# Kernel tuning notes

Measured on AMD Instinct MI355X. Metric: run time of the kernel, lower is better.

## Reference

```python
import jax, jax.numpy as jnp
import numpy as np

B, S, D = 2, 2048, 2048
H, KVH = 16, 4
HD = D // H  # 128
ROPE_BASE = 10000.0
EPS = 1e-6
QK_GAIN_INIT = 1.5


def _rms_norm(x):
    var = jnp.mean(jnp.square(x), axis=-1, keepdims=True)
    return x * jax.lax.rsqrt(var + EPS)


def _rope_tables(seqlen, head_dim, dtype):
    half = head_dim // 2
    inv_freq = 1.0 / (ROPE_BASE ** (jnp.arange(0, head_dim, 2, dtype=jnp.float32) / head_dim))
    freqs = jnp.outer(jnp.arange(seqlen, dtype=jnp.float32), inv_freq)  # [S, half]
    return jnp.cos(freqs).astype(dtype)[None, None], jnp.sin(freqs).astype(dtype)[None, None]


def _apply_rotary(x, cos, sin):
    half = x.shape[-1] // 2
    x1, x2 = x[..., :half], x[..., half:]
    return jnp.concatenate((x1 * cos + x2 * sin, -x1 * sin + x2 * cos), axis=-1)


def setup_inputs() -> dict:
    key = jax.random.key(0)
    ks = jax.random.split(key, 5)
    scale = 0.02
    return {
        "x": jax.random.normal(ks[0], (B, S, D), dtype=jnp.float32),
        "Wq": jax.random.normal(ks[1], (D, D), dtype=jnp.float32) * scale,
        "Wk": jax.random.normal(ks[2], (KVH * HD, D), dtype=jnp.float32) * scale,
        "Wv": jax.random.normal(ks[3], (KVH * HD, D), dtype=jnp.float32) * scale,
        "Wproj": jax.random.normal(ks[4], (D, D), dtype=jnp.float32) * scale,
        "q_gain": jnp.full((H,), QK_GAIN_INIT, dtype=jnp.float32),
    }


def reference(x, Wq, Wk, Wv, Wproj, q_gain):
    bsz, seqlen, dim = x.shape
    # QKV projections (torch Linear: y = x @ W.T)
    q = (x @ Wq.T).reshape(bsz, seqlen, H, HD).transpose(0, 2, 1, 3)      # [B,H,S,HD]
    k = (x @ Wk.T).reshape(bsz, seqlen, KVH, HD).transpose(0, 2, 1, 3)    # [B,KVH,S,HD]
    v = (x @ Wv.T).reshape(bsz, seqlen, KVH, HD).transpose(0, 2, 1, 3)
    # QK RMSNorm
    q = _rms_norm(q)
    k = _rms_norm(k)
    # RoPE
    cos, sin = _rope_tables(seqlen, HD, q.dtype)
    q = _apply_rotary(q, cos, sin)
    k = _apply_rotary(k, cos, sin)
    # per-head gain on q
    q = q * q_gain[None, :, None, None]
    # GQA: repeat k/v heads
    n_rep = H // KVH
    k = jnp.repeat(k, n_rep, axis=1)  # [B,H,S,HD]
    v = jnp.repeat(v, n_rep, axis=1)
    # causal SDPA, scale = 1/sqrt(head_dim)
    scores = jnp.einsum("bhqd,bhkd->bhqk", q, k) / jnp.sqrt(jnp.float32(HD))
    causal = jnp.tril(jnp.ones((seqlen, seqlen), dtype=bool))
    scores = jnp.where(causal[None, None], scores, jnp.finfo(scores.dtype).min)
    attn = jax.nn.softmax(scores, axis=-1)
    y = jnp.einsum("bhqk,bhkd->bhqd", attn, v)  # [B,H,S,HD]
    y = y.transpose(0, 2, 1, 3).reshape(bsz, seqlen, dim)
    return y @ Wproj.T
```

## Files before the change

### kernel.cpp

```cpp
#include <hip/hip_runtime.h>
#include <hip/hip_bf16.h>

typedef __attribute__((ext_vector_type(8))) short bf16x8;
typedef __attribute__((ext_vector_type(4))) short bf16x4;
typedef __attribute__((ext_vector_type(4))) float f32x4;
typedef unsigned short u16;

#define B_ 2
#define S_ 2048
#define H_ 16
#define KVH_ 4
#define HD_ 128

__device__ __forceinline__ float bf2f(u16 u) { return __uint_as_float(((unsigned)u) << 16); }
__device__ __forceinline__ u16 f2bf(float f) {
  __hip_bfloat16 h = __float2bfloat16(f);
  return *reinterpret_cast<u16*>(&h);
}
__device__ __forceinline__ void gld16(const void* g, void* l) {
  __builtin_amdgcn_global_load_lds((const __attribute__((address_space(1))) void*)g,
                                   (__attribute__((address_space(3))) void*)l, 16, 0, 0);
}

#define WAITV(n)                                                    \
  do {                                                              \
    asm volatile("s_waitcnt vmcnt(" #n ")" ::: "memory");           \
    __builtin_amdgcn_sched_barrier(0);                              \
  } while (0)

__global__ void detect_kernel(const u16* __restrict__ x, int* __restrict__ flag) {
  __shared__ int tot;
  if (threadIdx.x == 0) tot = 0;
  __syncthreads();
  int cnt = 0;
  for (int i = threadIdx.x; i < 16384; i += 256) {
    unsigned e = (x[i] >> 7) & 0xFF;
    if (e >= 160) cnt++;
  }
  atomicAdd(&tot, cnt);
  __syncthreads();
  if (threadIdx.x == 0) *flag = (tot >= 8) ? 1 : 0;
}

__global__ __launch_bounds__(256) void convert_all_kernel(
    const void* __restrict__ s0, const void* __restrict__ s1, const void* __restrict__ s2,
    const void* __restrict__ s3, const void* __restrict__ s4,
    u16* __restrict__ d0, u16* __restrict__ d1, u16* __restrict__ d2,
    u16* __restrict__ d3, u16* __restrict__ d4, const int* __restrict__ flag) {
  int bb = blockIdx.x;
  const void* src; u16* dst; int base;
  if (bb < 4096)      { src = s0; dst = d0; base = bb; }
  else if (bb < 6144) { src = s1; dst = d1; base = bb - 4096; }
  else if (bb < 6656) { src = s2; dst = d2; base = bb - 6144; }
  else if (bb < 7168) { src = s3; dst = d3; base = bb - 6656; }
  else                { src = s4; dst = d4; base = bb - 7168; }
  int i = (base * 256 + (int)threadIdx.x) * 8;
  if (*flag) {
    const float* s = (const float*)src;
    float4 a = *(const float4*)(s + i);
    float4 b = *(const float4*)(s + i + 4);
    ushort4 o0, o1;
    o0.x = f2bf(a.x); o0.y = f2bf(a.y); o0.z = f2bf(a.z); o0.w = f2bf(a.w);
    o1.x = f2bf(b.x); o1.y = f2bf(b.y); o1.z = f2bf(b.z); o1.w = f2bf(b.w);
    *(ushort4*)(dst + i) = o0;
    *(ushort4*)(dst + i + 4) = o1;
  } else {
    *(uint4*)(dst + i) = *(const uint4*)((const u16*)src + i);
  }
}

__device__ __forceinline__ void stage16(const u16* __restrict__ src, int row0, int K,
                                        int k0, u16* dst, int tid, int wave) {
#pragma unroll
  for (int s = 0; s < 2; ++s) {
    int f = s * 256 + tid, r = f >> 2, kk = (f & 3) << 3;
    gld16(&src[(size_t)(row0 + r) * K + k0 + kk], &dst[(size_t)(s * 256 + wave * 64) * 8]);
  }
}

__device__ __forceinline__ void mfma_tile(const u16* As, const u16* Bs, f32x4 acc[4][4],
                                          int wr, int wc, int l15, int quad) {
  bf16x8 af[4], bfr[4];
#pragma unroll
  for (int i = 0; i < 4; ++i)
    af[i] = *(const bf16x8*)(&As[(wr + i * 16 + l15) * 32 + quad * 8]);
#pragma unroll
  for (int j = 0; j < 4; ++j)
    bfr[j] = *(const bf16x8*)(&Bs[(wc + j * 16 + l15) * 32 + quad * 8]);
#pragma unroll
  for (int i = 0; i < 4; ++i)
#pragma unroll
    for (int j = 0; j < 4; ++j)
      acc[i][j] = __builtin_amdgcn_mfma_f32_16x16x32_bf16(af[i], bfr[j], acc[i][j], 0, 0, 0);
}

__device__ __forceinline__ void gemm_loop(const u16* __restrict__ A, const u16* __restrict__ W,
                                          int m0, int n0, int tid, int wave,
                                          int l15, int quad,
                                          u16* As0, u16* As1, u16* Bs0, u16* Bs1,
                                          f32x4 acc[4][4]) {
  const int wr = (wave >> 1) * 64, wc = (wave & 1) * 64;
  u16* Asb[2] = {As0, As1};
  u16* Bsb[2] = {Bs0, Bs1};
  stage16(A, m0, 2048, 0, As0, tid, wave);
  stage16(W, n0, 2048, 0, Bs0, tid, wave);
  for (int k0 = 0; k0 < 2048; k0 += 32) {
    int cur = (k0 >> 5) & 1;
    __syncthreads();
    if (k0 + 32 < 2048) {
      stage16(A, m0, 2048, k0 + 32, Asb[cur ^ 1], tid, wave);
      stage16(W, n0, 2048, k0 + 32, Bsb[cur ^ 1], tid, wave);
    }
    mfma_tile(Asb[cur], Bsb[cur], acc, wr, wc, l15, quad);
  }
}

__global__ __launch_bounds__(256) void gemm_qkv_kernel(
    const u16* __restrict__ x,
    const u16* __restrict__ Wq, const u16* __restrict__ Wk, const u16* __restrict__ Wv,
    u16* __restrict__ q, u16* __restrict__ k, u16* __restrict__ vt) {
  __shared__ __align__(16) u16 As[2][128 * 32];
  __shared__ __align__(16) u16 Bs[2][128 * 32];
  const int tid = threadIdx.x;
  const int lane = tid & 63, wave = tid >> 6;
  const int l15 = lane & 15, quad = lane >> 4;
  const int wr = (wave >> 1) * 64, wc = (wave & 1) * 64;
  const int tn = blockIdx.x;
  const int m0 = blockIdx.y * 128;
  const u16* Wp; int n0;
  if (tn < 16)      { Wp = Wq; n0 = tn * 128; }
  else if (tn < 20) { Wp = Wk; n0 = (tn - 16) * 128; }
  else              { Wp = Wv; n0 = (tn - 20) * 128; }

  f32x4 acc[4][4] = {};
  gemm_loop(x, Wp, m0, n0, tid, wave, l15, quad, As[0], As[1], Bs[0], Bs[1], acc);

  if (tn < 20) {
    u16* C = (tn < 16) ? q : k;
    int N = (tn < 16) ? 2048 : 512;
#pragma unroll
    for (int i = 0; i < 4; ++i)
#pragma unroll
      for (int j = 0; j < 4; ++j) {
        int row = m0 + wr + i * 16 + quad * 4;
        int col = n0 + wc + j * 16 + l15;
#pragma unroll
        for (int r = 0; r < 4; ++r)
          C[(size_t)(row + r) * N + col] = f2bf(acc[i][j][r]);
      }
  } else {
#pragma unroll
    for (int i = 0; i < 4; ++i)
#pragma unroll
      for (int j = 0; j < 4; ++j) {
        int row = m0 + wr + i * 16 + quad * 4;
        int col = n0 + wc + j * 16 + l15;
        int bb = row >> 11, ss = row & (S_ - 1);
        int kvh = col >> 7, d = col & (HD_ - 1);
        ushort4 pk;
        pk.x = f2bf(acc[i][j][0]); pk.y = f2bf(acc[i][j][1]);
        pk.z = f2bf(acc[i][j][2]); pk.w = f2bf(acc[i][j][3]);
        *(ushort4*)&vt[(((size_t)bb * KVH_ + kvh) * HD_ + d) * S_ + ss] = pk;
      }
  }
}

__global__ __launch_bounds__(256) void gemm_proj_kernel(
    const u16* __restrict__ A, const u16* __restrict__ Wp, void* __restrict__ outp,
    const int* __restrict__ flag) {
  __shared__ __align__(16) u16 As[2][128 * 32];
  __shared__ __align__(16) u16 Bs[2][128 * 32];
  const int tid = threadIdx.x;
  const int lane = tid & 63, wave = tid >> 6;
  const int l15 = lane & 15, quad = lane >> 4;
  const int wr = (wave >> 1) * 64, wc = (wave & 1) * 64;
  const int m0 = blockIdx.y * 128, n0 = blockIdx.x * 128;

  f32x4 acc[4][4] = {};
  gemm_loop(A, Wp, m0, n0, tid, wave, l15, quad, As[0], As[1], Bs[0], Bs[1], acc);

  const int fl = *flag;
#pragma unroll
  for (int i = 0; i < 4; ++i)
#pragma unroll
    for (int j = 0; j < 4; ++j) {
      int row = m0 + wr + i * 16 + quad * 4;
      int col = n0 + wc + j * 16 + l15;
      if (fl) {
        float* Cf = (float*)outp;
#pragma unroll
        for (int r = 0; r < 4; ++r) Cf[(size_t)(row + r) * 2048 + col] = acc[i][j][r];
      } else {
        u16* Cb = (u16*)outp;
#pragma unroll
        for (int r = 0; r < 4; ++r) Cb[(size_t)(row + r) * 2048 + col] = f2bf(acc[i][j][r]);
      }
    }
}

__global__ __launch_bounds__(256) void rope_rms_kernel(u16* __restrict__ x,
                                                       int rows, int nh,
                                                       const void* __restrict__ gain,
                                                       const int* __restrict__ flag) {
  const int fl = *flag;
  int row  = blockIdx.x * 4 + (threadIdx.x >> 6);
  int lane = threadIdx.x & 63;
  if (row >= rows) return;
  int h = row % nh;
  int s = (row / nh) & (S_ - 1);
  u16* p = x + (size_t)row * HD_;
  float x1 = bf2f(p[lane]);
  float x2 = bf2f(p[lane + 64]);
  float ss = x1 * x1 + x2 * x2;
#pragma unroll
  for (int m = 1; m < 64; m <<= 1) ss += __shfl_xor(ss, m, 64);
  float rn = rsqrtf(ss * (1.0f / 128.0f) + 1e-6f);
  x1 *= rn; x2 *= rn;
  float f = exp2f((float)lane * -0.20762050593046f);
  float ang = (float)s * f;
  float sn, cs;
  sincosf(ang, &sn, &cs);
  float o1 = x1 * cs + x2 * sn;
  float o2 = -x1 * sn + x2 * cs;
  if (gain) {
    float g = fl ? ((const float*)gain)[h] : bf2f(((const u16*)gain)[h]);
    o1 *= g; o2 *= g;
  }
  p[lane]      = f2bf(o1);
  p[lane + 64] = f2bf(o2);
}

#define C1_ 0.127517437f
#define C2_ 24.5258157f
__global__ __launch_bounds__(512, 4) void attn_kernel(const u16* __restrict__ Q,
                                                      const u16* __restrict__ Kg,
                                                      const u16* __restrict__ Vt,
                                                      u16* __restrict__ Y) {
  __shared__ __align__(16) u16 smem[32768];
#define KSm(bi) (smem + (size_t)(bi) * 8192)
#define Vsm     (smem + 16384)
#define PBv     ((bf16x4*)(smem + 24576))

  const int tid  = threadIdx.x;
  const int lane = tid & 63;
  const int wave = tid >> 6;
  const int l15  = lane & 15;
  const int quad = lane >> 4;
  const int T    = wave >> 2;
  const int qg   = wave & 3;

  const int i   = blockIdx.x;
  const int qt  = (i < 256) ? (31 - (i >> 4)) : ((i - 256) >> 4);
  const int id  = i & 15;
  const int b   = id >> 3;
  const int pr  = id & 7;
  const int h0  = pr * 2;
  const int kvh = pr >> 1;
  const int qglob = qt * 64 + qg * 16 + l15;

  bf16x8 qfA[4], qfB[4];
#pragma unroll
  for (int kb = 0; kb < 4; ++kb) {
    size_t base = ((size_t)(b * S_ + qglob) * H_ + h0) * HD_ + kb * 32 + quad * 8;
    qfA[kb] = *(const bf16x8*)&Q[base];
    qfB[kb] = *(const bf16x8*)&Q[base + HD_];
  }

  f32x4 yA[4] = {}, yB[4] = {};
  float lA = 0.f, lB = 0.f;

#define STAGE_K(jj, bi)                                                                  \
  {                                                                                      \
    int kv0p = (jj) * 64;                                                                \
    _Pragma("unroll") for (int it = 0; it < 2; ++it) {                                   \
      int c = it * 512 + tid, r = c >> 4, ccg = (c & 15) ^ (r & 15);                     \
      gld16(&Kg[((size_t)(b * S_ + kv0p + r) * KVH_ + kvh) * HD_ + ccg * 8],             \
            &KSm(bi)[(size_t)(it * 512 + wave * 64) * 8]);                               \
    }                                                                                    \
  }
#define STAGE_V(jj)                                                                      \
  {                                                                                      \
    int kv0p = (jj) * 64;                                                                \
    _Pragma("unroll") for (int it = 0; it < 2; ++it) {                                   \
      int c = it * 512 + tid, r = c >> 3, sg = (c & 7) ^ (r & 7);                        \
      gld16(&Vt[(((size_t)b * KVH_ + kvh) * HD_ + r) * S_ + kv0p + sg * 8],              \
            &Vsm[(size_t)(it * 512 + wave * 64) * 8]);                                   \
    }                                                                                    \
  }

#define PVCHUNK(nn, pa, pb)                                                              \
  {                                                                                      \
    _Pragma("unroll") for (int t = 0; t < 4; ++t) {                                      \
      int d = T * 64 + t * 16 + l15;                                                     \
      int chunk = (2 * (nn) + (quad >> 1)) ^ (d & 7);                                    \
      bf16x4 va = *(const bf16x4*)&Vsm[(size_t)(d * 8 + chunk) * 8 + (quad & 1) * 4];    \
      yA[t] = __builtin_amdgcn_mfma_f32_16x16x16bf16_1k(va, (pa), yA[t], 0, 0, 0);       \
      yB[t] = __builtin_amdgcn_mfma_f32_16x16x16bf16_1k(va, (pb), yB[t], 0, 0, 0);       \
    }                                                                                    \
  }

#define PIDX(half, m, h) ((((((half) * 4 + qg) * 2 + (m)) * 2 + (h)) * 64) + lane)

  STAGE_K(0, 0);

  for (int j = 0; j <= qt; ++j) {
    const int kv0 = j * 64;
    __syncthreads();
    STAGE_V(j);
    if (j < qt) STAGE_K(j + 1, (j + 1) & 1);
    const u16* Ksc = KSm(j & 1);

    const bool diag = (j == qt);
    bf16x4 pA[2], pB[2];
#pragma unroll
    for (int n = 0; n < 2; ++n) {
      f32x4 a = {0.f, 0.f, 0.f, 0.f}, c2 = {0.f, 0.f, 0.f, 0.f};
      int krow = T * 32 + n * 16 + l15;
      __builtin_amdgcn_s_setprio(1);
#pragma unroll
      for (int kb = 0; kb < 4; ++kb) {
        bf16x8 kf = *(const bf16x8*)&Ksc[krow * 128 + ((kb * 4 + quad) ^ l15) * 8];
        a  = __builtin_amdgcn_mfma_f32_16x16x32_bf16(kf, qfA[kb], a, 0, 0, 0);
        c2 = __builtin_amdgcn_mfma_f32_16x16x32_bf16(kf, qfB[kb], c2, 0, 0, 0);
      }
      __builtin_amdgcn_s_setprio(0);
      bf16x4 ta, tb;
      if (!diag) {
#pragma unroll
        for (int r = 0; r < 4; ++r) {
          float pa = exp2f(a[r] * C1_ - C2_);
          float pb = exp2f(c2[r] * C1_ - C2_);
          lA += pa; lB += pb;
          ta[r] = (short)f2bf(pa);
          tb[r] = (short)f2bf(pb);
        }
      } else {
#pragma unroll
        for (int r = 0; r < 4; ++r) {
          int kv = kv0 + T * 32 + n * 16 + quad * 4 + r;
          bool msk = (kv > qglob);
          float pa = msk ? 0.f : exp2f(a[r] * C1_ - C2_);
          float pb = msk ? 0.f : exp2f(c2[r] * C1_ - C2_);
          lA += pa; lB += pb;
          ta[r] = (short)f2bf(pa);
          tb[r] = (short)f2bf(pb);
        }
      }
      pA[n] = ta; pB[n] = tb;
    }

    PBv[PIDX(T, 0, 0)] = pA[0];
    PBv[PIDX(T, 0, 1)] = pB[0];
    PBv[PIDX(T, 1, 0)] = pA[1];
    PBv[PIDX(T, 1, 1)] = pB[1];

    if (j < qt) WAITV(2); else WAITV(0);
    asm volatile("s_waitcnt lgkmcnt(0)" ::: "memory");
    __builtin_amdgcn_sched_barrier(0);
    __builtin_amdgcn_s_barrier();
    __builtin_amdgcn_sched_barrier(0);

    __builtin_amdgcn_s_setprio(1);
    {
      int nown = T * 2;
      PVCHUNK(nown + 0, pA[0], pB[0]);
      PVCHUNK(nown + 1, pA[1], pB[1]);
      int npar = (1 - T) * 2;
      bf16x4 xa0 = PBv[PIDX(1 - T, 0, 0)];
      bf16x4 xb0 = PBv[PIDX(1 - T, 0, 1)];
      PVCHUNK(npar + 0, xa0, xb0);
      bf16x4 xa1 = PBv[PIDX(1 - T, 1, 0)];
      bf16x4 xb1 = PBv[PIDX(1 - T, 1, 1)];
      PVCHUNK(npar + 1, xa1, xb1);
    }
    __builtin_amdgcn_s_setprio(0);
  }

  __syncthreads();
  float* lb = (float*)PBv;
  lb[((T * 4 + qg) * 2 + 0) * 64 + lane] = lA;
  lb[((T * 4 + qg) * 2 + 1) * 64 + lane] = lB;
  __syncthreads();
  lA += lb[(((1 - T) * 4 + qg) * 2 + 0) * 64 + lane];
  lB += lb[(((1 - T) * 4 + qg) * 2 + 1) * 64 + lane];
  lA += __shfl_xor(lA, 16, 64); lA += __shfl_xor(lA, 32, 64);
  lB += __shfl_xor(lB, 16, 64); lB += __shfl_xor(lB, 32, 64);
  float ia = 1.0f / lA, ib = 1.0f / lB;
  size_t base = ((size_t)(b * S_ + qglob) * H_ + h0) * HD_;
#pragma unroll
  for (int t = 0; t < 4; ++t) {
    int d0 = T * 64 + t * 16 + quad * 4;
    ushort4 oa, ob;
    oa.x = f2bf(yA[t][0] * ia); oa.y = f2bf(yA[t][1] * ia);
    oa.z = f2bf(yA[t][2] * ia); oa.w = f2bf(yA[t][3] * ia);
    ob.x = f2bf(yB[t][0] * ib); ob.y = f2bf(yB[t][1] * ib);
    ob.z = f2bf(yB[t][2] * ib); ob.w = f2bf(yB[t][3] * ib);
    *(ushort4*)&Y[base + d0]       = oa;
    *(ushort4*)&Y[base + HD_ + d0] = ob;
  }
}

extern "C" void kernel_launch(void* const* d_in, const int* in_sizes, int n_in,
                              void* d_out, int out_size, void* d_ws, size_t ws_size,
                              hipStream_t stream) {
  u16* xb  = (u16*)d_ws;
  u16* Wqb = xb  + (size_t)8388608;
  u16* Wkb = Wqb + (size_t)4194304;
  u16* Wvb = Wkb + (size_t)1048576;
  u16* Wpb = Wvb + (size_t)1048576;
  u16* q   = Wpb + (size_t)4194304;
  u16* k   = q   + (size_t)8388608;
  u16* vt  = k   + (size_t)2097152;
  u16* y   = vt  + (size_t)2097152;
  int* flag = (int*)(y + (size_t)8388608);

  detect_kernel<<<1, 256, 0, stream>>>((const u16*)d_in[0], flag);
  convert_all_kernel<<<9216, 256, 0, stream>>>(d_in[0], d_in[1], d_in[2], d_in[3], d_in[4],
                                               xb, Wqb, Wkb, Wvb, Wpb, flag);

  gemm_qkv_kernel<<<dim3(24, 32), 256, 0, stream>>>(xb, Wqb, Wkb, Wvb, q, k, vt);
  rope_rms_kernel<<<65536 / 4, 256, 0, stream>>>(q, 65536, H_, d_in[5], flag);
  rope_rms_kernel<<<16384 / 4, 256, 0, stream>>>(k, 16384, KVH_, nullptr, flag);
  attn_kernel<<<512, 512, 0, stream>>>(q, k, vt, y);
  gemm_proj_kernel<<<dim3(16, 32), 256, 0, stream>>>(y, Wpb, d_out, flag);
}
```

Measured before the change: 328.1 us.

## Fuse QK RMSNorm and RoPE into QKV GEMM epilogue; fold dtype detection into convert

The QKV GEMM epilogue now applies the per-row RMS norm, RoPE rotation and q gain before writing q and k. This removes the two separate rope_rms passes that re-read and re-wrote q and k. The wave column mapping changes so each wave holds both rotary halves (d and d+64) of a head. A cross-wave sum of squares through shared memory completes each row's norm. The separate detect kernel is dropped: every convert block samples its own data to decide the input dtype, and block 0 writes the flag used by later kernels, which adds a block-wide sync and an extra read in the conversion.

```diff
diff --git a/kernel.cpp b/kernel.cpp
--- a/kernel.cpp
+++ b/kernel.cpp
@@ -28,25 +28,11 @@
     __builtin_amdgcn_sched_barrier(0);                              \
   } while (0)
 
-__global__ void detect_kernel(const u16* __restrict__ x, int* __restrict__ flag) {
-  __shared__ int tot;
-  if (threadIdx.x == 0) tot = 0;
-  __syncthreads();
-  int cnt = 0;
-  for (int i = threadIdx.x; i < 16384; i += 256) {
-    unsigned e = (x[i] >> 7) & 0xFF;
-    if (e >= 160) cnt++;
-  }
-  atomicAdd(&tot, cnt);
-  __syncthreads();
-  if (threadIdx.x == 0) *flag = (tot >= 8) ? 1 : 0;
-}
-
 __global__ __launch_bounds__(256) void convert_all_kernel(
     const void* __restrict__ s0, const void* __restrict__ s1, const void* __restrict__ s2,
     const void* __restrict__ s3, const void* __restrict__ s4,
     u16* __restrict__ d0, u16* __restrict__ d1, u16* __restrict__ d2,
-    u16* __restrict__ d3, u16* __restrict__ d4, const int* __restrict__ flag) {
+    u16* __restrict__ d3, u16* __restrict__ d4, int* __restrict__ flag) {
   int bb = blockIdx.x;
   const void* src; u16* dst; int base;
   if (bb < 4096)      { src = s0; dst = d0; base = bb; }
@@ -55,7 +41,26 @@
   else if (bb < 7168) { src = s3; dst = d3; base = bb - 6656; }
   else                { src = s4; dst = d4; base = bb - 7168; }
   int i = (base * 256 + (int)threadIdx.x) * 8;
-  if (*flag) {
+
+  __shared__ int tot;
+  if (threadIdx.x == 0) tot = 0;
+  __syncthreads();
+  {
+    uint4 smp = *(const uint4*)((const u16*)src + i);
+    unsigned w[4] = {smp.x, smp.y, smp.z, smp.w};
+    int c = 0;
+#pragma unroll
+    for (int t = 0; t < 4; ++t) {
+      c += (((w[t] >> 7)  & 0xFF) >= 160);
+      c += (((w[t] >> 23) & 0xFF) >= 160);
+    }
+    if (c) atomicAdd(&tot, c);
+  }
+  __syncthreads();
+  const int isf32 = (tot >= 8);
+  if (bb == 0 && threadIdx.x == 0) *flag = isf32;
+
+  if (isf32) {
     const float* s = (const float*)src;
     float4 a = *(const float4*)(s + i);
     float4 b = *(const float4*)(s + i + 4);
@@ -79,14 +84,14 @@
 }
 
 __device__ __forceinline__ void mfma_tile(const u16* As, const u16* Bs, f32x4 acc[4][4],
-                                          int wr, int wc, int l15, int quad) {
+                                          int wr, int wc2, int l15, int quad) {
   bf16x8 af[4], bfr[4];
 #pragma unroll
   for (int i = 0; i < 4; ++i)
     af[i] = *(const bf16x8*)(&As[(wr + i * 16 + l15) * 32 + quad * 8]);
 #pragma unroll
   for (int j = 0; j < 4; ++j)
-    bfr[j] = *(const bf16x8*)(&Bs[(wc + j * 16 + l15) * 32 + quad * 8]);
+    bfr[j] = *(const bf16x8*)(&Bs[(wc2 + (j >> 1) * 64 + (j & 1) * 16 + l15) * 32 + quad * 8]);
 #pragma unroll
   for (int i = 0; i < 4; ++i)
 #pragma unroll
@@ -99,7 +104,7 @@
                                           int l15, int quad,
                                           u16* As0, u16* As1, u16* Bs0, u16* Bs1,
                                           f32x4 acc[4][4]) {
-  const int wr = (wave >> 1) * 64, wc = (wave & 1) * 64;
+  const int wr = (wave >> 1) * 64, wc2 = (wave & 1) * 32;
   u16* Asb[2] = {As0, As1};
   u16* Bsb[2] = {Bs0, Bs1};
   stage16(A, m0, 2048, 0, As0, tid, wave);
@@ -111,20 +116,21 @@
       stage16(A, m0, 2048, k0 + 32, Asb[cur ^ 1], tid, wave);
       stage16(W, n0, 2048, k0 + 32, Bsb[cur ^ 1], tid, wave);
     }
-    mfma_tile(Asb[cur], Bsb[cur], acc, wr, wc, l15, quad);
+    mfma_tile(Asb[cur], Bsb[cur], acc, wr, wc2, l15, quad);
   }
 }
 
 __global__ __launch_bounds__(256) void gemm_qkv_kernel(
     const u16* __restrict__ x,
     const u16* __restrict__ Wq, const u16* __restrict__ Wk, const u16* __restrict__ Wv,
-    u16* __restrict__ q, u16* __restrict__ k, u16* __restrict__ vt) {
+    u16* __restrict__ q, u16* __restrict__ k, u16* __restrict__ vt,
+    const void* __restrict__ gain, const int* __restrict__ flag) {
   __shared__ __align__(16) u16 As[2][128 * 32];
   __shared__ __align__(16) u16 Bs[2][128 * 32];
   const int tid = threadIdx.x;
   const int lane = tid & 63, wave = tid >> 6;
   const int l15 = lane & 15, quad = lane >> 4;
-  const int wr = (wave >> 1) * 64, wc = (wave & 1) * 64;
+  const int wr = (wave >> 1) * 64, wc2 = (wave & 1) * 32;
   const int tn = blockIdx.x;
   const int m0 = blockIdx.y * 128;
   const u16* Wp; int n0;
@@ -136,25 +142,51 @@
   gemm_loop(x, Wp, m0, n0, tid, wave, l15, quad, As[0], As[1], Bs[0], Bs[1], acc);
 
   if (tn < 20) {
-    u16* C = (tn < 16) ? q : k;
-    int N = (tn < 16) ? 2048 : 512;
+    __syncthreads();
+    float* sb = (float*)As;
+#pragma unroll
+    for (int i = 0; i < 4; ++i)
+#pragma unroll
+      for (int r = 0; r < 4; ++r) {
+        float ss = acc[i][0][r] * acc[i][0][r] + acc[i][1][r] * acc[i][1][r]
+                 + acc[i][2][r] * acc[i][2][r] + acc[i][3][r] * acc[i][3][r];
+        ss += __shfl_xor(ss, 1, 64); ss += __shfl_xor(ss, 2, 64);
+        ss += __shfl_xor(ss, 4, 64); ss += __shfl_xor(ss, 8, 64);
+        if (l15 == 0) sb[(wr + i * 16 + quad * 4 + r) * 2 + (wave & 1)] = ss;
+      }
+    __syncthreads();
+    float g = 1.0f;
+    if (tn < 16) g = (*flag) ? ((const float*)gain)[tn] : bf2f(((const u16*)gain)[tn]);
+    u16* C  = (tn < 16) ? q : k;
+    int  CN = (tn < 16) ? 2048 : 512;
+    int  c0 = (tn < 16) ? tn * 128 : (tn - 16) * 128;
+#pragma unroll
+    for (int i = 0; i < 4; ++i)
+#pragma unroll
+      for (int r = 0; r < 4; ++r) {
+        int rl = wr + i * 16 + quad * 4 + r;
+        float rn = rsqrtf((sb[rl * 2] + sb[rl * 2 + 1]) * (1.0f / 128.0f) + 1e-6f) * g;
+        int grow = m0 + rl;
+        int s = grow & (S_ - 1);
+#pragma unroll
+        for (int j = 0; j < 2; ++j) {
+          int p = wc2 + j * 16 + l15;
+          float f = exp2f((float)p * -0.20762050593046f);
+          float sn, cs;
+          sincosf((float)s * f, &sn, &cs);
+          float x1 = acc[i][j][r] * rn;
+          float x2 = acc[i][j + 2][r] * rn;
+          C[(size_t)grow * CN + c0 + p]      = f2bf(x1 * cs + x2 * sn);
+          C[(size_t)grow * CN + c0 + p + 64] = f2bf(x2 * cs - x1 * sn);
+        }
+      }
+  } else {
 #pragma unroll
     for (int i = 0; i < 4; ++i)
 #pragma unroll
       for (int j = 0; j < 4; ++j) {
         int row = m0 + wr + i * 16 + quad * 4;
-        int col = n0 + wc + j * 16 + l15;
-#pragma unroll
-        for (int r = 0; r < 4; ++r)
-          C[(size_t)(row + r) * N + col] = f2bf(acc[i][j][r]);
-      }
-  } else {
-#pragma unroll
-    for (int i = 0; i < 4; ++i)
-#pragma unroll
-      for (int j = 0; j < 4; ++j) {
-        int row = m0 + wr + i * 16 + quad * 4;
-        int col = n0 + wc + j * 16 + l15;
+        int col = n0 + wc2 + (j >> 1) * 64 + (j & 1) * 16 + l15;
         int bb = row >> 11, ss = row & (S_ - 1);
         int kvh = col >> 7, d = col & (HD_ - 1);
         ushort4 pk;
@@ -173,7 +205,7 @@
   const int tid = threadIdx.x;
   const int lane = tid & 63, wave = tid >> 6;
   const int l15 = lane & 15, quad = lane >> 4;
-  const int wr = (wave >> 1) * 64, wc = (wave & 1) * 64;
+  const int wr = (wave >> 1) * 64, wc2 = (wave & 1) * 32;
   const int m0 = blockIdx.y * 128, n0 = blockIdx.x * 128;
 
   f32x4 acc[4][4] = {};
@@ -185,7 +217,7 @@
 #pragma unroll
     for (int j = 0; j < 4; ++j) {
       int row = m0 + wr + i * 16 + quad * 4;
-      int col = n0 + wc + j * 16 + l15;
+      int col = n0 + wc2 + (j >> 1) * 64 + (j & 1) * 16 + l15;
       if (fl) {
         float* Cf = (float*)outp;
 #pragma unroll
@@ -196,38 +228,6 @@
         for (int r = 0; r < 4; ++r) Cb[(size_t)(row + r) * 2048 + col] = f2bf(acc[i][j][r]);
       }
     }
-}
-
-__global__ __launch_bounds__(256) void rope_rms_kernel(u16* __restrict__ x,
-                                                       int rows, int nh,
-                                                       const void* __restrict__ gain,
-                                                       const int* __restrict__ flag) {
-  const int fl = *flag;
-  int row  = blockIdx.x * 4 + (threadIdx.x >> 6);
-  int lane = threadIdx.x & 63;
-  if (row >= rows) return;
-  int h = row % nh;
-  int s = (row / nh) & (S_ - 1);
-  u16* p = x + (size_t)row * HD_;
-  float x1 = bf2f(p[lane]);
-  float x2 = bf2f(p[lane + 64]);
-  float ss = x1 * x1 + x2 * x2;
-#pragma unroll
-  for (int m = 1; m < 64; m <<= 1) ss += __shfl_xor(ss, m, 64);
-  float rn = rsqrtf(ss * (1.0f / 128.0f) + 1e-6f);
-  x1 *= rn; x2 *= rn;
-  float f = exp2f((float)lane * -0.20762050593046f);
-  float ang = (float)s * f;
-  float sn, cs;
-  sincosf(ang, &sn, &cs);
-  float o1 = x1 * cs + x2 * sn;
-  float o2 = -x1 * sn + x2 * cs;
-  if (gain) {
-    float g = fl ? ((const float*)gain)[h] : bf2f(((const u16*)gain)[h]);
-    o1 *= g; o2 *= g;
-  }
-  p[lane]      = f2bf(o1);
-  p[lane + 64] = f2bf(o2);
 }
 
 #define C1_ 0.127517437f
@@ -414,13 +414,10 @@
   u16* y   = vt  + (size_t)2097152;
   int* flag = (int*)(y + (size_t)8388608);
 
-  detect_kernel<<<1, 256, 0, stream>>>((const u16*)d_in[0], flag);
   convert_all_kernel<<<9216, 256, 0, stream>>>(d_in[0], d_in[1], d_in[2], d_in[3], d_in[4],
                                                xb, Wqb, Wkb, Wvb, Wpb, flag);
-
-  gemm_qkv_kernel<<<dim3(24, 32), 256, 0, stream>>>(xb, Wqb, Wkb, Wvb, q, k, vt);
-  rope_rms_kernel<<<65536 / 4, 256, 0, stream>>>(q, 65536, H_, d_in[5], flag);
-  rope_rms_kernel<<<16384 / 4, 256, 0, stream>>>(k, 16384, KVH_, nullptr, flag);
+  gemm_qkv_kernel<<<dim3(24, 32), 256, 0, stream>>>(xb, Wqb, Wkb, Wvb, q, k, vt,
+                                                    d_in[5], flag);
   attn_kernel<<<512, 512, 0, stream>>>(q, k, vt, y);
   gemm_proj_kernel<<<dim3(16, 32), 256, 0, stream>>>(y, Wpb, d_out, flag);
 }
```

New measurement: 337.0 us. 2.7% more time.
